# Performance work log

Hardware: AMD Instinct MI355X
Metric: run time of the kernel (lower is better)

Reference implementation:

```python
import jax, jax.numpy as jnp
import numpy as np

T, B, I, H, O = 256, 128, 512, 1024, 1


def setup_inputs() -> dict:
    key = jax.random.key(0)
    ks = jax.random.split(key, 7)
    s_ih = 1.0 / np.sqrt(H)
    return {
        "x": jax.random.normal(ks[0], (T, B, I), dtype=jnp.float32),
        "W_ih": jax.random.normal(ks[1], (H, I), dtype=jnp.float32) * s_ih,
        "W_hh": jax.random.normal(ks[2], (H, H), dtype=jnp.float32) * s_ih,
        "b_ih": jax.random.normal(ks[3], (H,), dtype=jnp.float32) * s_ih,
        "b_hh": jax.random.normal(ks[4], (H,), dtype=jnp.float32) * s_ih,
        "W_fc": jax.random.normal(ks[5], (O, H), dtype=jnp.float32) * s_ih,
        "b_fc": jax.random.normal(ks[6], (O,), dtype=jnp.float32) * s_ih,
    }


def reference(x, W_ih, W_hh, b_ih, b_hh, W_fc, b_fc):
    # Precompute the input projection for all timesteps at once: [T, B, H]
    xp = jnp.einsum("tbi,hi->tbh", x, W_ih) + b_ih + b_hh
    W_hh_T = W_hh.T  # [H, H]

    def step(h, xp_t):
        # h: [B, H]; torch nn.RNN uses tanh nonlinearity by default
        h_new = jnp.tanh(xp_t + h @ W_hh_T)
        return h_new, h_new

    h0 = jnp.zeros((B, H), dtype=x.dtype)  # hidden0 = zeros in the module
    _, hs = jax.lax.scan(step, h0, xp)  # hs: [T, B, H]

    # Linear head over every timestep's hidden state: [T, B, O]
    return jnp.einsum("tbh,oh->tbo", hs, W_fc) + b_fc
```

## Files before the change

kernel.cpp:

```cpp
#include <hip/hip_runtime.h>
#include <stdint.h>

typedef __attribute__((ext_vector_type(8))) short short8;
typedef __attribute__((ext_vector_type(4))) float f32x4;
typedef __attribute__((ext_vector_type(4))) unsigned int u32x4;
typedef __attribute__((ext_vector_type(2))) unsigned int u32x2;

__device__ __forceinline__ unsigned short f2bf(float f) {
  unsigned u = __float_as_uint(f);
  u += 0x7FFFu + ((u >> 16) & 1u);
  return (unsigned short)(u >> 16);
}
__device__ __forceinline__ float bf2f(unsigned short s) {
  return __uint_as_float(((unsigned)s) << 16);
}
__device__ __forceinline__ float ftanh(float x) {
  float e = __expf(2.0f * x);
  return 1.0f - 2.0f / (e + 1.0f);
}

__global__ __launch_bounds__(256) void cvt_kernel(const float* __restrict__ in,
                                                  unsigned short* __restrict__ out,
                                                  int n8) {
  int i = blockIdx.x * 256 + threadIdx.x;
  if (i >= n8) return;
  const float4* p = (const float4*)in + (size_t)i * 2;
  float4 a = p[0], b = p[1];
  uint4 o;
  o.x = (unsigned)f2bf(a.x) | ((unsigned)f2bf(a.y) << 16);
  o.y = (unsigned)f2bf(a.z) | ((unsigned)f2bf(a.w) << 16);
  o.z = (unsigned)f2bf(b.x) | ((unsigned)f2bf(b.y) << 16);
  o.w = (unsigned)f2bf(b.z) | ((unsigned)f2bf(b.w) << 16);
  ((uint4*)out)[i] = o;
}

__global__ __launch_bounds__(256) void scrub_kernel(unsigned* __restrict__ dst,
                                                    int n4) {
  int i = blockIdx.x * 256 + threadIdx.x;
  if (i >= n4) return;
  ((u32x4*)dst)[i] = (u32x4){0xAAAAAAAAu, 0xAAAAAAAAu, 0xAAAAAAAAu, 0xAAAAAAAAu};
}

__global__ __launch_bounds__(256) void gemm_xp(const unsigned short* __restrict__ A,
                                               const unsigned short* __restrict__ Bw,
                                               const float* __restrict__ b_ih,
                                               const float* __restrict__ b_hh,
                                               unsigned short* __restrict__ xp) {
  __shared__ unsigned short Al[8192];
  __shared__ unsigned short Bl[8192];
  int tid = threadIdx.x, lane = tid & 63, w = tid >> 6;
  int wm = w & 1, wn = w >> 1;
  int bx = blockIdx.x;
  int m0 = (bx >> 3) * 128, n0 = (bx & 7) * 128;

  f32x4 acc[4][4];
#pragma unroll
  for (int i = 0; i < 4; ++i)
#pragma unroll
    for (int jq = 0; jq < 4; ++jq) acc[i][jq] = (f32x4){0.f, 0.f, 0.f, 0.f};

  for (int kb = 0; kb < 512; kb += 64) {
#pragma unroll
    for (int i = 0; i < 4; ++i) {
      int S = (w * 4 + i) * 64 + lane;
      int row = S >> 3, pg = S & 7;
      int gk = ((pg ^ (row & 7)) << 3);
      const unsigned short* ga = A + (size_t)(m0 + row) * 512 + kb + gk;
      const unsigned short* gb = Bw + (size_t)(n0 + row) * 512 + kb + gk;
      __builtin_amdgcn_global_load_lds(
          (const __attribute__((address_space(1))) unsigned int*)ga,
          (__attribute__((address_space(3))) unsigned int*)&Al[(size_t)((w * 4 + i) * 64) * 8],
          16, 0, 0);
      __builtin_amdgcn_global_load_lds(
          (const __attribute__((address_space(1))) unsigned int*)gb,
          (__attribute__((address_space(3))) unsigned int*)&Bl[(size_t)((w * 4 + i) * 64) * 8],
          16, 0, 0);
    }
    asm volatile("s_waitcnt vmcnt(0)" ::: "memory");
    __syncthreads();

#pragma unroll
    for (int c = 0; c < 2; ++c) {
      short8 av[4], bv[4];
      int gg = c * 4 + (lane >> 4);
#pragma unroll
      for (int mt = 0; mt < 4; ++mt) {
        int rowa = wm * 64 + mt * 16 + (lane & 15);
        av[mt] = *(const short8*)&Al[(rowa * 8 + (gg ^ (rowa & 7))) * 8];
        int rowb = wn * 64 + mt * 16 + (lane & 15);
        bv[mt] = *(const short8*)&Bl[(rowb * 8 + (gg ^ (rowb & 7))) * 8];
      }
#pragma unroll
      for (int mt = 0; mt < 4; ++mt)
#pragma unroll
        for (int nt = 0; nt < 4; ++nt)
          acc[mt][nt] = __builtin_amdgcn_mfma_f32_16x16x32_bf16(av[mt], bv[nt], acc[mt][nt], 0, 0, 0);
    }
    __syncthreads();
  }

  int cl = lane & 15, qd = lane >> 4;
#pragma unroll
  for (int nt = 0; nt < 4; ++nt) {
    int col = n0 + wn * 64 + nt * 16 + cl;
    float bias = b_ih[col] + b_hh[col];
#pragma unroll
    for (int mt = 0; mt < 4; ++mt) {
#pragma unroll
      for (int r = 0; r < 4; ++r) {
        int m = m0 + wm * 64 + mt * 16 + qd * 4 + r;
        xp[(size_t)m * 1024 + col] = f2bf(acc[mt][nt][r] + bias);
      }
    }
  }
}

__global__ __launch_bounds__(512, 1) void scan_kernel(
    const float* __restrict__ Whh, const unsigned short* __restrict__ xp,
    const float* __restrict__ Wfc, const float* __restrict__ bfc,
    unsigned short* __restrict__ hs, float* __restrict__ out) {
  __shared__ __align__(16) unsigned short Abuf[2][2048 * 8];
  const int tid = threadIdx.x;
  const int lane = tid & 63, w = tid >> 6;
  const int g = blockIdx.x >> 3, p = blockIdx.x & 7;
  const int r = lane & 15, q = lane >> 4;
  const int b0 = g * 16;
  const int tile = p * 128 + w * 16;
  const int gcol = tile + r;
  const float bfcv = bfc[0];
  const float4 wfc4 = *(const float4*)(Wfc + tile + q * 4);
  const unsigned short* xlane = xp + (size_t)(b0 + r) * 1024 + tile + q * 4;

  short8 Wf[32];
  {
    const float* wsrc = Whh + (size_t)gcol * 1024 + q * 8;
#pragma unroll
    for (int c = 0; c < 32; ++c) {
      float4 v0 = *(const float4*)(wsrc + c * 32);
      float4 v1 = *(const float4*)(wsrc + c * 32 + 4);
      short8 sv;
      sv[0] = (short)f2bf(v0.x); sv[1] = (short)f2bf(v0.y);
      sv[2] = (short)f2bf(v0.z); sv[3] = (short)f2bf(v0.w);
      sv[4] = (short)f2bf(v1.x); sv[5] = (short)f2bf(v1.y);
      sv[6] = (short)f2bf(v1.z); sv[7] = (short)f2bf(v1.w);
      Wf[c] = sv;
    }
  }

  {
#pragma unroll
    for (int i = 0; i < 4; ++i) {
      int m = tid + i * 512;
      int l = m & 63, c = m >> 6;
      int bb = l & 15, q2 = l >> 4;
      const unsigned short* src = xp + (size_t)(b0 + bb) * 1024 + c * 32 + q2 * 8;
      u32x4 xv = *(const u32x4*)src;
      const unsigned short* xs = (const unsigned short*)&xv;
      short8 sv;
      float pp = 0.f;
#pragma unroll
      for (int jj = 0; jj < 8; ++jj) {
        float h = ftanh(bf2f(xs[jj]));
        sv[jj] = (short)f2bf(h);
        pp += h * Wfc[c * 32 + q2 * 8 + jj];
      }
      *(short8*)&Abuf[1][(size_t)m * 8] = sv;
      if (p == 0) {
        if (m < 16) pp += bfcv;
        atomicAdd(out + b0 + bb, pp);
      }
    }
  }
  uint2 xw_next = *(const uint2*)(xlane + (size_t)1 * 131072);
  __syncthreads();

  for (int s = 1; s < 256; ++s) {
    uint2 xw = xw_next;
    {
      int sn = (s < 255) ? s + 1 : 255;
      xw_next = *(const uint2*)(xlane + (size_t)sn * 131072);
    }

    unsigned short* curA = Abuf[s & 1];
    if (s >= 2) {
      const unsigned short* hbase = hs + (size_t)(s - 1) * 131072;
      u32x4 v0, v1, v2, v3;
      const u32x4 *s0, *s1, *s2, *s3;
      {
        int m, l, c, bb, q2;
        m = tid;           l = m & 63; c = m >> 6; bb = l & 15; q2 = l >> 4;
        s0 = (const u32x4*)(hbase + (size_t)(b0 + bb) * 1024 + c * 32 + q2 * 8);
        m = tid + 512;     l = m & 63; c = m >> 6; bb = l & 15; q2 = l >> 4;
        s1 = (const u32x4*)(hbase + (size_t)(b0 + bb) * 1024 + c * 32 + q2 * 8);
        m = tid + 1024;    l = m & 63; c = m >> 6; bb = l & 15; q2 = l >> 4;
        s2 = (const u32x4*)(hbase + (size_t)(b0 + bb) * 1024 + c * 32 + q2 * 8);
        m = tid + 1536;    l = m & 63; c = m >> 6; bb = l & 15; q2 = l >> 4;
        s3 = (const u32x4*)(hbase + (size_t)(b0 + bb) * 1024 + c * 32 + q2 * 8);
      }
      v0 = *s0; v1 = *s1; v2 = *s2; v3 = *s3;
      const unsigned P = 0xAAAAAAAAu;
      int need =
          (v0[0] == P) | (v0[1] == P) | (v0[2] == P) | (v0[3] == P) |
          (v1[0] == P) | (v1[1] == P) | (v1[2] == P) | (v1[3] == P) |
          (v2[0] == P) | (v2[1] == P) | (v2[2] == P) | (v2[3] == P) |
          (v3[0] == P) | (v3[1] == P) | (v3[2] == P) | (v3[3] == P);
      int guard = 0;
      while (need) {
        asm volatile(
            "global_load_dwordx4 %0, %4, off sc1\n\t"
            "global_load_dwordx4 %1, %5, off sc1\n\t"
            "global_load_dwordx4 %2, %6, off sc1\n\t"
            "global_load_dwordx4 %3, %7, off sc1\n\t"
            "s_waitcnt vmcnt(0)"
            : "=&v"(v0), "=&v"(v1), "=&v"(v2), "=&v"(v3)
            : "v"((unsigned long long)(uintptr_t)s0),
              "v"((unsigned long long)(uintptr_t)s1),
              "v"((unsigned long long)(uintptr_t)s2),
              "v"((unsigned long long)(uintptr_t)s3)
            : "memory");
        need =
            (v0[0] == P) | (v0[1] == P) | (v0[2] == P) | (v0[3] == P) |
            (v1[0] == P) | (v1[1] == P) | (v1[2] == P) | (v1[3] == P) |
            (v2[0] == P) | (v2[1] == P) | (v2[2] == P) | (v2[3] == P) |
            (v3[0] == P) | (v3[1] == P) | (v3[2] == P) | (v3[3] == P);
        if (++guard > (1 << 18)) break;
      }
      *(u32x4*)&curA[(size_t)(tid) * 8]          = v0;
      *(u32x4*)&curA[(size_t)(tid + 512) * 8]    = v1;
      *(u32x4*)&curA[(size_t)(tid + 1024) * 8]   = v2;
      *(u32x4*)&curA[(size_t)(tid + 1536) * 8]   = v3;
      __syncthreads();
    }

    f32x4 acc0 = (f32x4){0.f, 0.f, 0.f, 0.f};
    f32x4 acc1 = (f32x4){0.f, 0.f, 0.f, 0.f};
#pragma unroll
    for (int c = 0; c < 16; ++c) {
      short8 a0 = *(const short8*)&curA[(size_t)(2 * c) * 512 + lane * 8];
      short8 a1 = *(const short8*)&curA[(size_t)(2 * c + 1) * 512 + lane * 8];
      acc0 = __builtin_amdgcn_mfma_f32_16x16x32_bf16(Wf[2 * c], a0, acc0, 0, 0, 0);
      acc1 = __builtin_amdgcn_mfma_f32_16x16x32_bf16(Wf[2 * c + 1], a1, acc1, 0, 0, 0);
    }

    float h0 = ftanh(acc0[0] + acc1[0] + bf2f((unsigned short)(xw.x & 0xffff)));
    float h1 = ftanh(acc0[1] + acc1[1] + bf2f((unsigned short)(xw.x >> 16)));
    float h2 = ftanh(acc0[2] + acc1[2] + bf2f((unsigned short)(xw.y & 0xffff)));
    float h3 = ftanh(acc0[3] + acc1[3] + bf2f((unsigned short)(xw.y >> 16)));
    u32x2 dv;
    dv[0] = (unsigned)f2bf(h0) | ((unsigned)f2bf(h1) << 16);
    dv[1] = (unsigned)f2bf(h2) | ((unsigned)f2bf(h3) << 16);
    unsigned long long pa = (unsigned long long)(uintptr_t)(
        hs + ((size_t)s * 128 + b0 + r) * 1024 + tile + q * 4);
    asm volatile("global_store_dwordx2 %0, %1, off sc1"
                 :: "v"(pa), "v"(dv) : "memory");

    float pp = h0 * wfc4.x + h1 * wfc4.y + h2 * wfc4.z + h3 * wfc4.w;
    pp += __shfl_xor(pp, 16, 64);
    pp += __shfl_xor(pp, 32, 64);
    if (lane < 16) {
      if (p == 0 && w == 0) pp += bfcv;
      atomicAdd(out + (size_t)s * 128 + b0 + lane, pp);
    }
  }
}

extern "C" void kernel_launch(void* const* d_in, const int* in_sizes, int n_in,
                              void* d_out, int out_size, void* d_ws, size_t ws_size,
                              hipStream_t stream) {
  (void)in_sizes; (void)n_in;
  const float* x   = (const float*)d_in[0];
  const float* Wih = (const float*)d_in[1];
  const float* Whh = (const float*)d_in[2];
  const float* bih = (const float*)d_in[3];
  const float* bhh = (const float*)d_in[4];
  const float* Wfc = (const float*)d_in[5];
  const float* bfc = (const float*)d_in[6];
  float* out = (float*)d_out;

  char* ws = (char*)d_ws;
  const bool big = ws_size >= (size_t)168820736;
  unsigned short* xp = (unsigned short*)(ws);
  unsigned short* hs = (unsigned short*)(ws + 67108864);
  unsigned short* xb = big ? (unsigned short*)(ws + 134217728)
                           : (unsigned short*)(ws + 67108864);
  unsigned short* wb = big ? (unsigned short*)(ws + 167772160)
                           : (unsigned short*)(ws + 100663296);

  hipMemsetAsync(out, 0, (size_t)out_size * 4, stream);

  cvt_kernel<<<8192, 256, 0, stream>>>(x, xb, 2097152);
  cvt_kernel<<<256, 256, 0, stream>>>(Wih, wb, 65536);
  gemm_xp<<<2048, 256, 0, stream>>>(xb, wb, bih, bhh, xp);
  if (!big) {
    scrub_kernel<<<8384, 256, 0, stream>>>(
        (unsigned*)(ws + 67108864 + 262144), 2146304);
  }
  scan_kernel<<<64, 512, 0, stream>>>(Whh, xp, Wfc, bfc, hs, out);
}
```

Before: 987.9 us.

## Interleave two batch strips per block in RNN scan to hide cross-block latency

Each scan block now owns two 16-row batch strips and processes them back to back within every timestep, reusing the register-resident W_hh fragment for both. The grid halves from 64 to 32 blocks. The goal is to overlap the global-memory polling for one strip's previous hidden state with the other strip's matrix work, and to cut the number of blocks contending in the handoff. The trade-off is doubled serial work per block per step and fewer CUs used, which could lengthen the per-step critical path.

Measured after the change: 1.576 ms. +59.6%, slower.

```diff
diff --git a/kernel.cpp b/kernel.cpp
--- a/kernel.cpp
+++ b/kernel.cpp
@@ -115,21 +115,73 @@
   }
 }
 
+__device__ __forceinline__ void stage_strip(const unsigned short* __restrict__ hbase,
+                                            int b0, int tid,
+                                            unsigned short* __restrict__ buf) {
+  u32x4 v0, v1, v2, v3;
+  const u32x4 *s0, *s1, *s2, *s3;
+  {
+    int m, l, c, bb, q2;
+    m = tid;           l = m & 63; c = m >> 6; bb = l & 15; q2 = l >> 4;
+    s0 = (const u32x4*)(hbase + (size_t)(b0 + bb) * 1024 + c * 32 + q2 * 8);
+    m = tid + 512;     l = m & 63; c = m >> 6; bb = l & 15; q2 = l >> 4;
+    s1 = (const u32x4*)(hbase + (size_t)(b0 + bb) * 1024 + c * 32 + q2 * 8);
+    m = tid + 1024;    l = m & 63; c = m >> 6; bb = l & 15; q2 = l >> 4;
+    s2 = (const u32x4*)(hbase + (size_t)(b0 + bb) * 1024 + c * 32 + q2 * 8);
+    m = tid + 1536;    l = m & 63; c = m >> 6; bb = l & 15; q2 = l >> 4;
+    s3 = (const u32x4*)(hbase + (size_t)(b0 + bb) * 1024 + c * 32 + q2 * 8);
+  }
+  v0 = *s0; v1 = *s1; v2 = *s2; v3 = *s3;
+  const unsigned P = 0xAAAAAAAAu;
+  int need =
+      (v0[0] == P) | (v0[1] == P) | (v0[2] == P) | (v0[3] == P) |
+      (v1[0] == P) | (v1[1] == P) | (v1[2] == P) | (v1[3] == P) |
+      (v2[0] == P) | (v2[1] == P) | (v2[2] == P) | (v2[3] == P) |
+      (v3[0] == P) | (v3[1] == P) | (v3[2] == P) | (v3[3] == P);
+  int guard = 0;
+  while (need) {
+    asm volatile(
+        "global_load_dwordx4 %0, %4, off sc1\n\t"
+        "global_load_dwordx4 %1, %5, off sc1\n\t"
+        "global_load_dwordx4 %2, %6, off sc1\n\t"
+        "global_load_dwordx4 %3, %7, off sc1\n\t"
+        "s_waitcnt vmcnt(0)"
+        : "=&v"(v0), "=&v"(v1), "=&v"(v2), "=&v"(v3)
+        : "v"((unsigned long long)(uintptr_t)s0),
+          "v"((unsigned long long)(uintptr_t)s1),
+          "v"((unsigned long long)(uintptr_t)s2),
+          "v"((unsigned long long)(uintptr_t)s3)
+        : "memory");
+    need =
+        (v0[0] == P) | (v0[1] == P) | (v0[2] == P) | (v0[3] == P) |
+        (v1[0] == P) | (v1[1] == P) | (v1[2] == P) | (v1[3] == P) |
+        (v2[0] == P) | (v2[1] == P) | (v2[2] == P) | (v2[3] == P) |
+        (v3[0] == P) | (v3[1] == P) | (v3[2] == P) | (v3[3] == P);
+    if (++guard > (1 << 18)) break;
+  }
+  *(u32x4*)&buf[(size_t)(tid) * 8]          = v0;
+  *(u32x4*)&buf[(size_t)(tid + 512) * 8]    = v1;
+  *(u32x4*)&buf[(size_t)(tid + 1024) * 8]   = v2;
+  *(u32x4*)&buf[(size_t)(tid + 1536) * 8]   = v3;
+}
+
 __global__ __launch_bounds__(512, 1) void scan_kernel(
     const float* __restrict__ Whh, const unsigned short* __restrict__ xp,
     const float* __restrict__ Wfc, const float* __restrict__ bfc,
     unsigned short* __restrict__ hs, float* __restrict__ out) {
-  __shared__ __align__(16) unsigned short Abuf[2][2048 * 8];
+  __shared__ __align__(16) unsigned short AbufA[2048 * 8];
+  __shared__ __align__(16) unsigned short AbufB[2048 * 8];
   const int tid = threadIdx.x;
   const int lane = tid & 63, w = tid >> 6;
-  const int g = blockIdx.x >> 3, p = blockIdx.x & 7;
+  const int gp = blockIdx.x >> 3, p = blockIdx.x & 7;
   const int r = lane & 15, q = lane >> 4;
-  const int b0 = g * 16;
+  const int b0A = gp * 32, b0B = gp * 32 + 16;
   const int tile = p * 128 + w * 16;
   const int gcol = tile + r;
   const float bfcv = bfc[0];
   const float4 wfc4 = *(const float4*)(Wfc + tile + q * 4);
-  const unsigned short* xlane = xp + (size_t)(b0 + r) * 1024 + tile + q * 4;
+  const unsigned short* xlaneA = xp + (size_t)(b0A + r) * 1024 + tile + q * 4;
+  const unsigned short* xlaneB = xp + (size_t)(b0B + r) * 1024 + tile + q * 4;
 
   short8 Wf[32];
   {
@@ -147,7 +199,10 @@
     }
   }
 
-  {
+#pragma unroll
+  for (int ctx = 0; ctx < 2; ++ctx) {
+    const int b0 = ctx ? b0B : b0A;
+    unsigned short* buf = ctx ? AbufB : AbufA;
 #pragma unroll
     for (int i = 0; i < 4; ++i) {
       int m = tid + i * 512;
@@ -164,102 +219,90 @@
         sv[jj] = (short)f2bf(h);
         pp += h * Wfc[c * 32 + q2 * 8 + jj];
       }
-      *(short8*)&Abuf[1][(size_t)m * 8] = sv;
+      *(short8*)&buf[(size_t)m * 8] = sv;
       if (p == 0) {
         if (m < 16) pp += bfcv;
         atomicAdd(out + b0 + bb, pp);
       }
     }
   }
-  uint2 xw_next = *(const uint2*)(xlane + (size_t)1 * 131072);
+  uint2 xwA_next = *(const uint2*)(xlaneA + (size_t)131072);
+  uint2 xwB_next = *(const uint2*)(xlaneB + (size_t)131072);
   __syncthreads();
 
   for (int s = 1; s < 256; ++s) {
-    uint2 xw = xw_next;
+    const unsigned short* hbase = hs + (size_t)(s - 1) * 131072;
+    uint2 xwA = xwA_next;
     {
       int sn = (s < 255) ? s + 1 : 255;
-      xw_next = *(const uint2*)(xlane + (size_t)sn * 131072);
-    }
-
-    unsigned short* curA = Abuf[s & 1];
-    if (s >= 2) {
-      const unsigned short* hbase = hs + (size_t)(s - 1) * 131072;
-      u32x4 v0, v1, v2, v3;
-      const u32x4 *s0, *s1, *s2, *s3;
-      {
-        int m, l, c, bb, q2;
-        m = tid;           l = m & 63; c = m >> 6; bb = l & 15; q2 = l >> 4;
-        s0 = (const u32x4*)(hbase + (size_t)(b0 + bb) * 1024 + c * 32 + q2 * 8);
-        m = tid + 512;     l = m & 63; c = m >> 6; bb = l & 15; q2 = l >> 4;
-        s1 = (const u32x4*)(hbase + (size_t)(b0 + bb) * 1024 + c * 32 + q2 * 8);
-        m = tid + 1024;    l = m & 63; c = m >> 6; bb = l & 15; q2 = l >> 4;
-        s2 = (const u32x4*)(hbase + (size_t)(b0 + bb) * 1024 + c * 32 + q2 * 8);
-        m = tid + 1536;    l = m & 63; c = m >> 6; bb = l & 15; q2 = l >> 4;
-        s3 = (const u32x4*)(hbase + (size_t)(b0 + bb) * 1024 + c * 32 + q2 * 8);
-      }
-      v0 = *s0; v1 = *s1; v2 = *s2; v3 = *s3;
-      const unsigned P = 0xAAAAAAAAu;
-      int need =
-          (v0[0] == P) | (v0[1] == P) | (v0[2] == P) | (v0[3] == P) |
-          (v1[0] == P) | (v1[1] == P) | (v1[2] == P) | (v1[3] == P) |
-          (v2[0] == P) | (v2[1] == P) | (v2[2] == P) | (v2[3] == P) |
-          (v3[0] == P) | (v3[1] == P) | (v3[2] == P) | (v3[3] == P);
-      int guard = 0;
-      while (need) {
-        asm volatile(
-            "global_load_dwordx4 %0, %4, off sc1\n\t"
-            "global_load_dwordx4 %1, %5, off sc1\n\t"
-            "global_load_dwordx4 %2, %6, off sc1\n\t"
-            "global_load_dwordx4 %3, %7, off sc1\n\t"
-            "s_waitcnt vmcnt(0)"
-            : "=&v"(v0), "=&v"(v1), "=&v"(v2), "=&v"(v3)
-            : "v"((unsigned long long)(uintptr_t)s0),
-              "v"((unsigned long long)(uintptr_t)s1),
-              "v"((unsigned long long)(uintptr_t)s2),
-              "v"((unsigned long long)(uintptr_t)s3)
-            : "memory");
-        need =
-            (v0[0] == P) | (v0[1] == P) | (v0[2] == P) | (v0[3] == P) |
-            (v1[0] == P) | (v1[1] == P) | (v1[2] == P) | (v1[3] == P) |
-            (v2[0] == P) | (v2[1] == P) | (v2[2] == P) | (v2[3] == P) |
-            (v3[0] == P) | (v3[1] == P) | (v3[2] == P) | (v3[3] == P);
-        if (++guard > (1 << 18)) break;
-      }
-      *(u32x4*)&curA[(size_t)(tid) * 8]          = v0;
-      *(u32x4*)&curA[(size_t)(tid + 512) * 8]    = v1;
-      *(u32x4*)&curA[(size_t)(tid + 1024) * 8]   = v2;
-      *(u32x4*)&curA[(size_t)(tid + 1536) * 8]   = v3;
-      __syncthreads();
-    }
-
-    f32x4 acc0 = (f32x4){0.f, 0.f, 0.f, 0.f};
-    f32x4 acc1 = (f32x4){0.f, 0.f, 0.f, 0.f};
-#pragma unroll
-    for (int c = 0; c < 16; ++c) {
-      short8 a0 = *(const short8*)&curA[(size_t)(2 * c) * 512 + lane * 8];
-      short8 a1 = *(const short8*)&curA[(size_t)(2 * c + 1) * 512 + lane * 8];
-      acc0 = __builtin_amdgcn_mfma_f32_16x16x32_bf16(Wf[2 * c], a0, acc0, 0, 0, 0);
-      acc1 = __builtin_amdgcn_mfma_f32_16x16x32_bf16(Wf[2 * c + 1], a1, acc1, 0, 0, 0);
-    }
-
-    float h0 = ftanh(acc0[0] + acc1[0] + bf2f((unsigned short)(xw.x & 0xffff)));
-    float h1 = ftanh(acc0[1] + acc1[1] + bf2f((unsigned short)(xw.x >> 16)));
-    float h2 = ftanh(acc0[2] + acc1[2] + bf2f((unsigned short)(xw.y & 0xffff)));
-    float h3 = ftanh(acc0[3] + acc1[3] + bf2f((unsigned short)(xw.y >> 16)));
-    u32x2 dv;
-    dv[0] = (unsigned)f2bf(h0) | ((unsigned)f2bf(h1) << 16);
-    dv[1] = (unsigned)f2bf(h2) | ((unsigned)f2bf(h3) << 16);
-    unsigned long long pa = (unsigned long long)(uintptr_t)(
-        hs + ((size_t)s * 128 + b0 + r) * 1024 + tile + q * 4);
-    asm volatile("global_store_dwordx2 %0, %1, off sc1"
-                 :: "v"(pa), "v"(dv) : "memory");
-
-    float pp = h0 * wfc4.x + h1 * wfc4.y + h2 * wfc4.z + h3 * wfc4.w;
-    pp += __shfl_xor(pp, 16, 64);
-    pp += __shfl_xor(pp, 32, 64);
-    if (lane < 16) {
-      if (p == 0 && w == 0) pp += bfcv;
-      atomicAdd(out + (size_t)s * 128 + b0 + lane, pp);
+      xwA_next = *(const uint2*)(xlaneA + (size_t)sn * 131072);
+    }
+    if (s >= 2) stage_strip(hbase, b0A, tid, AbufA);
+    __syncthreads();
+    {
+      f32x4 acc0 = (f32x4){0.f, 0.f, 0.f, 0.f};
+      f32x4 acc1 = (f32x4){0.f, 0.f, 0.f, 0.f};
+#pragma unroll
+      for (int c = 0; c < 16; ++c) {
+        short8 a0 = *(const short8*)&AbufA[(size_t)(2 * c) * 512 + lane * 8];
+        short8 a1 = *(const short8*)&AbufA[(size_t)(2 * c + 1) * 512 + lane * 8];
+        acc0 = __builtin_amdgcn_mfma_f32_16x16x32_bf16(Wf[2 * c], a0, acc0, 0, 0, 0);
+        acc1 = __builtin_amdgcn_mfma_f32_16x16x32_bf16(Wf[2 * c + 1], a1, acc1, 0, 0, 0);
+      }
+      float h0 = ftanh(acc0[0] + acc1[0] + bf2f((unsigned short)(xwA.x & 0xffff)));
+      float h1 = ftanh(acc0[1] + acc1[1] + bf2f((unsigned short)(xwA.x >> 16)));
+      float h2 = ftanh(acc0[2] + acc1[2] + bf2f((unsigned short)(xwA.y & 0xffff)));
+      float h3 = ftanh(acc0[3] + acc1[3] + bf2f((unsigned short)(xwA.y >> 16)));
+      u32x2 dv;
+      dv[0] = (unsigned)f2bf(h0) | ((unsigned)f2bf(h1) << 16);
+      dv[1] = (unsigned)f2bf(h2) | ((unsigned)f2bf(h3) << 16);
+      unsigned long long pa = (unsigned long long)(uintptr_t)(
+          hs + ((size_t)s * 128 + b0A + r) * 1024 + tile + q * 4);
+      asm volatile("global_store_dwordx2 %0, %1, off sc1"
+                   :: "v"(pa), "v"(dv) : "memory");
+      float pp = h0 * wfc4.x + h1 * wfc4.y + h2 * wfc4.z + h3 * wfc4.w;
+      pp += __shfl_xor(pp, 16, 64);
+      pp += __shfl_xor(pp, 32, 64);
+      if (lane < 16) {
+        if (p == 0 && w == 0) pp += bfcv;
+        atomicAdd(out + (size_t)s * 128 + b0A + lane, pp);
+      }
+    }
+    uint2 xwB = xwB_next;
+    {
+      int sn = (s < 255) ? s + 1 : 255;
+      xwB_next = *(const uint2*)(xlaneB + (size_t)sn * 131072);
+    }
+    if (s >= 2) stage_strip(hbase, b0B, tid, AbufB);
+    __syncthreads();
+    {
+      f32x4 acc0 = (f32x4){0.f, 0.f, 0.f, 0.f};
+      f32x4 acc1 = (f32x4){0.f, 0.f, 0.f, 0.f};
+#pragma unroll
+      for (int c = 0; c < 16; ++c) {
+        short8 a0 = *(const short8*)&AbufB[(size_t)(2 * c) * 512 + lane * 8];
+        short8 a1 = *(const short8*)&AbufB[(size_t)(2 * c + 1) * 512 + lane * 8];
+        acc0 = __builtin_amdgcn_mfma_f32_16x16x32_bf16(Wf[2 * c], a0, acc0, 0, 0, 0);
+        acc1 = __builtin_amdgcn_mfma_f32_16x16x32_bf16(Wf[2 * c + 1], a1, acc1, 0, 0, 0);
+      }
+      float h0 = ftanh(acc0[0] + acc1[0] + bf2f((unsigned short)(xwB.x & 0xffff)));
+      float h1 = ftanh(acc0[1] + acc1[1] + bf2f((unsigned short)(xwB.x >> 16)));
+      float h2 = ftanh(acc0[2] + acc1[2] + bf2f((unsigned short)(xwB.y & 0xffff)));
+      float h3 = ftanh(acc0[3] + acc1[3] + bf2f((unsigned short)(xwB.y >> 16)));
+      u32x2 dv;
+      dv[0] = (unsigned)f2bf(h0) | ((unsigned)f2bf(h1) << 16);
+      dv[1] = (unsigned)f2bf(h2) | ((unsigned)f2bf(h3) << 16);
+      unsigned long long pa = (unsigned long long)(uintptr_t)(
+          hs + ((size_t)s * 128 + b0B + r) * 1024 + tile + q * 4);
+      asm volatile("global_store_dwordx2 %0, %1, off sc1"
+                   :: "v"(pa), "v"(dv) : "memory");
+      float pp = h0 * wfc4.x + h1 * wfc4.y + h2 * wfc4.z + h3 * wfc4.w;
+      pp += __shfl_xor(pp, 16, 64);
+      pp += __shfl_xor(pp, 32, 64);
+      if (lane < 16) {
+        if (p == 0 && w == 0) pp += bfcv;
+        atomicAdd(out + (size_t)s * 128 + b0B + lane, pp);
+      }
     }
   }
 }
@@ -295,5 +338,5 @@
     scrub_kernel<<<8384, 256, 0, stream>>>(
         (unsigned*)(ws + 67108864 + 262144), 2146304);
   }
-  scan_kernel<<<64, 512, 0, stream>>>(Whh, xp, Wfc, bfc, hs, out);
-}
+  scan_kernel<<<32, 512, 0, stream>>>(Whh, xp, Wfc, bfc, hs, out);
+}
```
